# Optimization experiments

Measured on AMD Instinct MI355X. Metric: run time of the kernel, lower is better.

Reference implementation:

```python
import jax, jax.numpy as jnp
import numpy as np

B, S, D, H, P = 4, 512, 512, 8, 16
DK = D // H  # 64


def setup_inputs() -> dict:
    k0 = jax.random.key(0)
    ks = jax.random.split(k0, 10)
    std = 0.02
    lin = lambda k, shape: jax.random.normal(k, shape, dtype=jnp.float32) * std
    inp = {}
    inp["query"] = jax.random.normal(ks[0], (B, S, D), dtype=jnp.float32)
    inp["key"] = jax.random.normal(ks[1], (B, S, D), dtype=jnp.float32)
    inp["value"] = jax.random.normal(ks[2], (B, S, D), dtype=jnp.float32)
    inp["Wq"] = lin(ks[3], (D, D)); inp["bq"] = jnp.zeros((D,), jnp.float32)
    inp["Wk"] = lin(ks[4], (D, D)); inp["bk"] = jnp.zeros((D,), jnp.float32)
    inp["Wv"] = lin(ks[5], (D, D)); inp["bv"] = jnp.zeros((D,), jnp.float32)
    inp["Wo"] = lin(ks[6], (D, D)); inp["bo"] = jnp.zeros((D,), jnp.float32)
    inp["rel_table"] = lin(ks[7], (2 * P + 1, DK))  # nn.Embedding(2P+1, d_k)
    inp["gamma"] = jnp.ones((D,), jnp.float32)
    inp["beta"] = jnp.zeros((D,), jnp.float32)
    inp["mask"] = jnp.ones((B, S), dtype=jnp.int32)
    inp["relative_positions"] = jax.random.randint(ks[8], (B, S, S, DK), -32, 33, dtype=jnp.int32)
    return inp


def reference(query, key, value, Wq, bq, Wk, bk, Wv, bv, Wo, bo, rel_table, gamma, beta, mask, relative_positions):
    b, s, d = query.shape
    dk = rel_table.shape[1]
    h = d // dk
    pmax = (rel_table.shape[0] - 1) // 2

    def heads(x, W, bias):
        return (x @ W.T + bias).reshape(b, s, h, dk).transpose(0, 2, 1, 3)  # [b,h,s,dk]

    Q = heads(query, Wq, bq)
    K = heads(key, Wk, bk)
    V = heads(value, Wv, bv)

    scores = jnp.einsum('bhid,bhjd->bhij', Q, K) / jnp.sqrt(jnp.float32(dk))

    # torch: einsum('bhid,bijde->bhije', Q, emb(idx)).mean(-1)
    # mean over e commutes with the d-contraction -> pre-average the table.
    idx = jnp.clip(relative_positions, -pmax, pmax) + pmax  # [b,i,j,d]
    bias_d = rel_table.mean(axis=-1)[idx]                   # [b,i,j,d]
    scores = scores + jnp.einsum('bhid,bijd->bhij', Q, bias_d)

    scores = jnp.where(mask[:, None, None, :] == 0, jnp.float32(-1e9), scores)
    attn = jax.nn.softmax(scores, axis=-1)  # dropout is identity in eval

    ctx = jnp.einsum('bhij,bhjd->bhid', attn, V).transpose(0, 2, 1, 3).reshape(b, s, d)
    out = ctx @ Wo.T + bo

    x = out + query  # residual
    mu = x.mean(-1, keepdims=True)
    var = x.var(-1, keepdims=True)
    y = (x - mu) / jnp.sqrt(var + 1e-5) * gamma + beta
    return (y, attn)
```

## Files before the change

### kernel.cpp

```cpp
#include <hip/hip_runtime.h>
#include <hip/hip_bf16.h>

#define BB 4
#define SS 512
#define DD 512
#define HH 8
#define DK 64
#define PP 16
#define TSZ 33

typedef __bf16 bf16x8 __attribute__((ext_vector_type(8)));
typedef float  f32x4  __attribute__((ext_vector_type(4)));

__device__ inline bf16x8 cvt8(const float* __restrict__ p) {
    f32x4 a = *(const f32x4*)p;
    f32x4 b = *(const f32x4*)(p + 4);
    bf16x8 r;
    r[0] = (__bf16)a[0]; r[1] = (__bf16)a[1]; r[2] = (__bf16)a[2]; r[3] = (__bf16)a[3];
    r[4] = (__bf16)b[0]; r[5] = (__bf16)b[1]; r[6] = (__bf16)b[2]; r[7] = (__bf16)b[3];
    return r;
}

__global__ void tmean_kernel(const float* __restrict__ rel_table, float* __restrict__ Tm) {
    int t = threadIdx.x;
    if (t < TSZ) {
        float s = 0.f;
        for (int e = 0; e < DK; ++e) s += rel_table[t * DK + e];
        Tm[t] = s * (1.f / DK);
    }
}

__global__ void proj_mfma_kernel(const float* __restrict__ X, const float* __restrict__ W,
                                 const float* __restrict__ bias, __bf16* __restrict__ out,
                                 int mode) {
    int lane = threadIdx.x;
    int wave = threadIdx.y;
    int tm = blockIdx.y * 4 + wave;
    int tn = blockIdx.x;
    int m = lane & 15, quad = lane >> 4;

    const float* arow = X + (size_t)(tm * 16 + m) * DD + quad * 8;
    const float* brow = W + (size_t)(tn * 16 + m) * DD + quad * 8;

    f32x4 acc = {0.f, 0.f, 0.f, 0.f};
    for (int k0 = 0; k0 < DD; k0 += 32) {
        bf16x8 a = cvt8(arow + k0);
        bf16x8 b = cvt8(brow + k0);
        acc = __builtin_amdgcn_mfma_f32_16x16x32_bf16(a, b, acc, 0, 0, 0);
    }

    int col = tn * 16 + m;
    int h = col >> 6, dk = col & (DK - 1);
    float bv = bias[col];
#pragma unroll
    for (int r = 0; r < 4; ++r) {
        int rowg = tm * 16 + quad * 4 + r;
        int b = rowg >> 9, i = rowg & (SS - 1);
        float v = acc[r] + bv;
        if (mode == 0)
            out[((size_t)(b * HH + h) * SS + i) * DK + dk] = (__bf16)v;
        else
            out[((size_t)(b * HH + h) * DK + dk) * SS + i] = (__bf16)v;
    }
}

__global__ void scores_mfma_kernel(const __bf16* __restrict__ Q, const __bf16* __restrict__ K,
                                   float* __restrict__ scores) {
    int bh = blockIdx.z;
    int lane = threadIdx.x, wave = threadIdx.y;
    int tm = blockIdx.y * 4 + wave;
    int tn = blockIdx.x;
    int m = lane & 15, quad = lane >> 4;

    const __bf16* qrow = Q + ((size_t)bh * SS + tm * 16 + m) * DK + quad * 8;
    const __bf16* krow = K + ((size_t)bh * SS + tn * 16 + m) * DK + quad * 8;

    f32x4 acc = {0.f, 0.f, 0.f, 0.f};
#pragma unroll
    for (int k0 = 0; k0 < DK; k0 += 32) {
        bf16x8 a = *(const bf16x8*)(qrow + k0);
        bf16x8 b = *(const bf16x8*)(krow + k0);
        acc = __builtin_amdgcn_mfma_f32_16x16x32_bf16(a, b, acc, 0, 0, 0);
    }

    int col = tn * 16 + m;
#pragma unroll
    for (int r = 0; r < 4; ++r) {
        int rowg = tm * 16 + quad * 4 + r;
        scores[((size_t)bh * SS + rowg) * SS + col] = acc[r] * 0.125f;
    }
}

__global__ void relbias_kernel(const __bf16* __restrict__ Q, const int* __restrict__ relpos,
                               const float* __restrict__ Tm, float* __restrict__ scores) {
    int b = blockIdx.z;
    int i = blockIdx.y;
    int j0 = blockIdx.x * 64;
    __shared__ float tmean[TSZ];
    __shared__ float qrow[DD];
    int t = threadIdx.x;
    if (t < TSZ) tmean[t] = Tm[t];
    for (int o = t; o < DD; o += 256) {
        int h = o >> 6, d = o & (DK - 1);
        qrow[o] = (float)Q[((size_t)(b * HH + h) * SS + i) * DK + d];
    }
    __syncthreads();
    int jl = t >> 2, qq = t & 3;
    int j = j0 + jl;
    const int4* ip4 = (const int4*)(relpos + (((size_t)(b * SS + i) * SS + j) * DK) + qq * 16);
    int4 w0 = ip4[0], w1 = ip4[1], w2 = ip4[2], w3 = ip4[3];
    int rr[16] = {w0.x, w0.y, w0.z, w0.w, w1.x, w1.y, w1.z, w1.w,
                  w2.x, w2.y, w2.z, w2.w, w3.x, w3.y, w3.z, w3.w};
    float tv[16];
#pragma unroll
    for (int kk = 0; kk < 16; ++kk) {
        int r = min(max(rr[kk], -PP), PP) + PP;
        tv[kk] = tmean[r];
    }
#pragma unroll
    for (int h = 0; h < HH; ++h) {
        float p = 0.f;
#pragma unroll
        for (int kk = 0; kk < 16; ++kk) p += qrow[h * DK + qq * 16 + kk] * tv[kk];
        p += __shfl_xor(p, 1);
        p += __shfl_xor(p, 2);
        if (qq == 0) scores[((size_t)(b * HH + h) * SS + i) * SS + j] += p;
    }
}

__global__ void softmax_kernel(float* __restrict__ attn, const int* __restrict__ mask) {
    int bhi = blockIdx.x;
    int b = bhi >> 12;
    float* row = attn + (size_t)bhi * SS;
    int t = threadIdx.x;
    float v0 = row[t];
    float v1 = row[t + 256];
    if (mask[b * SS + t] == 0) v0 = -1e9f;
    if (mask[b * SS + t + 256] == 0) v1 = -1e9f;

    __shared__ float red[4];
    float m = fmaxf(v0, v1);
#pragma unroll
    for (int off = 32; off >= 1; off >>= 1) m = fmaxf(m, __shfl_xor(m, off));
    if ((t & 63) == 0) red[t >> 6] = m;
    __syncthreads();
    float mall = fmaxf(fmaxf(red[0], red[1]), fmaxf(red[2], red[3]));
    __syncthreads();

    float e0 = expf(v0 - mall);
    float e1 = expf(v1 - mall);
    float s = e0 + e1;
#pragma unroll
    for (int off = 32; off >= 1; off >>= 1) s += __shfl_xor(s, off);
    if ((t & 63) == 0) red[t >> 6] = s;
    __syncthreads();
    float sall = red[0] + red[1] + red[2] + red[3];
    float inv = 1.f / sall;
    row[t] = e0 * inv;
    row[t + 256] = e1 * inv;
}

__global__ void ctx_mfma_kernel(const float* __restrict__ attn, const __bf16* __restrict__ Vt,
                                __bf16* __restrict__ ctx_bsd) {
    int bh = blockIdx.z;
    int bb = bh >> 3, h = bh & 7;
    int lane = threadIdx.x, wave = threadIdx.y;
    int tm = blockIdx.y * 4 + wave;
    int tn = blockIdx.x;
    int m = lane & 15, quad = lane >> 4;

    const float*  arow = attn + ((size_t)bh * SS + tm * 16 + m) * SS + quad * 8;
    const __bf16* brow = Vt + ((size_t)bh * DK + tn * 16 + m) * SS + quad * 8;

    f32x4 acc = {0.f, 0.f, 0.f, 0.f};
    for (int k0 = 0; k0 < SS; k0 += 32) {
        bf16x8 a = cvt8(arow + k0);
        bf16x8 b = *(const bf16x8*)(brow + k0);
        acc = __builtin_amdgcn_mfma_f32_16x16x32_bf16(a, b, acc, 0, 0, 0);
    }

    int d = tn * 16 + m;
#pragma unroll
    for (int r = 0; r < 4; ++r) {
        int i = tm * 16 + quad * 4 + r;
        ctx_bsd[((size_t)(bb * SS + i)) * DD + h * DK + d] = (__bf16)acc[r];
    }
}

__global__ void outproj_mfma_kernel(const __bf16* __restrict__ Xc, const float* __restrict__ Wo,
                                    const float* __restrict__ bo, const float* __restrict__ query,
                                    float* __restrict__ xres) {
    int lane = threadIdx.x, wave = threadIdx.y;
    int tm = blockIdx.y * 4 + wave;
    int tn = blockIdx.x;
    int m = lane & 15, quad = lane >> 4;

    const __bf16* arow = Xc + (size_t)(tm * 16 + m) * DD + quad * 8;
    const float*  brow = Wo + (size_t)(tn * 16 + m) * DD + quad * 8;

    f32x4 acc = {0.f, 0.f, 0.f, 0.f};
    for (int k0 = 0; k0 < DD; k0 += 32) {
        bf16x8 a = *(const bf16x8*)(arow + k0);
        bf16x8 b = cvt8(brow + k0);
        acc = __builtin_amdgcn_mfma_f32_16x16x32_bf16(a, b, acc, 0, 0, 0);
    }

    int col = tn * 16 + m;
    float bv = bo[col];
#pragma unroll
    for (int r = 0; r < 4; ++r) {
        int rowg = tm * 16 + quad * 4 + r;
        xres[(size_t)rowg * DD + col] = acc[r] + bv + query[(size_t)rowg * DD + col];
    }
}

__global__ void ln_kernel(const float* __restrict__ x, const float* __restrict__ gamma,
                          const float* __restrict__ beta, float* __restrict__ y) {
    int r = blockIdx.x;
    int t = threadIdx.x;
    float v0 = x[r * DD + t];
    float v1 = x[r * DD + t + 256];
    __shared__ float red[4];
    float s = v0 + v1;
#pragma unroll
    for (int off = 32; off >= 1; off >>= 1) s += __shfl_xor(s, off);
    if ((t & 63) == 0) red[t >> 6] = s;
    __syncthreads();
    float mu = (red[0] + red[1] + red[2] + red[3]) * (1.f / DD);
    __syncthreads();
    float d0 = v0 - mu, d1 = v1 - mu;
    float sq = d0 * d0 + d1 * d1;
#pragma unroll
    for (int off = 32; off >= 1; off >>= 1) sq += __shfl_xor(sq, off);
    if ((t & 63) == 0) red[t >> 6] = sq;
    __syncthreads();
    float var = (red[0] + red[1] + red[2] + red[3]) * (1.f / DD);
    float inv = rsqrtf(var + 1e-5f);
    y[r * DD + t] = d0 * inv * gamma[t] + beta[t];
    y[r * DD + t + 256] = d1 * inv * gamma[t + 256] + beta[t + 256];
}

extern "C" void kernel_launch(void* const* d_in, const int* in_sizes, int n_in,
                              void* d_out, int out_size, void* d_ws, size_t ws_size,
                              hipStream_t stream) {
    const float* query  = (const float*)d_in[0];
    const float* key    = (const float*)d_in[1];
    const float* value  = (const float*)d_in[2];
    const float* Wq     = (const float*)d_in[3];
    const float* bq     = (const float*)d_in[4];
    const float* Wk     = (const float*)d_in[5];
    const float* bk     = (const float*)d_in[6];
    const float* Wv     = (const float*)d_in[7];
    const float* bv     = (const float*)d_in[8];
    const float* Wo     = (const float*)d_in[9];
    const float* bo     = (const float*)d_in[10];
    const float* rtab   = (const float*)d_in[11];
    const float* gamma  = (const float*)d_in[12];
    const float* beta   = (const float*)d_in[13];
    const int*   mask   = (const int*)d_in[14];
    const int*   relpos = (const int*)d_in[15];

    float* out = (float*)d_out;
    float* y    = out;
    float* attn = out + (size_t)BB * SS * DD;

    char* wsb = (char*)d_ws;
    float*  Tm    = (float*)wsb;                       wsb += 256;
    __bf16* Qbf   = (__bf16*)wsb;                      wsb += (size_t)BB * HH * SS * DK * 2;
    __bf16* Kbf   = (__bf16*)wsb;                      wsb += (size_t)BB * HH * SS * DK * 2;
    __bf16* Vtbf  = (__bf16*)wsb;                      wsb += (size_t)BB * HH * DK * SS * 2;
    __bf16* ctxbf = (__bf16*)wsb;                      wsb += (size_t)BB * SS * DD * 2;
    float*  xres  = (float*)wsb;                       wsb += (size_t)BB * SS * DD * 4;

    hipLaunchKernelGGL(tmean_kernel, dim3(1), dim3(64), 0, stream, rtab, Tm);

    dim3 wblk(64, 4);
    dim3 gproj(DD / 16, (BB * SS) / 64);
    hipLaunchKernelGGL(proj_mfma_kernel, gproj, wblk, 0, stream, query, Wq, bq, Qbf, 0);
    hipLaunchKernelGGL(proj_mfma_kernel, gproj, wblk, 0, stream, key,   Wk, bk, Kbf, 0);
    hipLaunchKernelGGL(proj_mfma_kernel, gproj, wblk, 0, stream, value, Wv, bv, Vtbf, 1);

    hipLaunchKernelGGL(scores_mfma_kernel, dim3(SS / 16, SS / 64, BB * HH), wblk, 0, stream,
                       Qbf, Kbf, attn);

    hipLaunchKernelGGL(relbias_kernel, dim3(SS / 64, SS, BB), dim3(256), 0, stream,
                       Qbf, relpos, Tm, attn);

    hipLaunchKernelGGL(softmax_kernel, dim3(BB * HH * SS), dim3(256), 0, stream, attn, mask);

    hipLaunchKernelGGL(ctx_mfma_kernel, dim3(DK / 16, SS / 64, BB * HH), wblk, 0, stream,
                       attn, Vtbf, ctxbf);

    hipLaunchKernelGGL(outproj_mfma_kernel, gproj, wblk, 0, stream, ctxbf, Wo, bo, query, xres);

    hipLaunchKernelGGL(ln_kernel, dim3(BB * SS), dim3(256), 0, stream, xres, gamma, beta, y);
}
```

Measured before the change: 581.0 us.

## Fuse scores, relative bias, mask and partial softmax; fuse normalize with context GEMM

Merges the three Q/K/V projection launches into one grid over z. Scores, the relative-position bias (relpos gathered through LDS), masking and a per-128-column partial softmax now run in one kernel that writes unnormalized exponentials plus per-chunk max and sum. A second kernel combines the partial statistics, rescales and writes the attention rows, and feeds them from LDS into the attention-times-V MFMA. This removes several full read-modify-write passes over the large scores tensor. In exchange it adds extra synchronisation, heavy LDS use, and the bias dot products now use bf16 table values.

```diff
diff --git a/kernel.cpp b/kernel.cpp
--- a/kernel.cpp
+++ b/kernel.cpp
@@ -10,6 +10,7 @@
 #define TSZ 33
 
 typedef __bf16 bf16x8 __attribute__((ext_vector_type(8)));
+typedef __bf16 bf16x4 __attribute__((ext_vector_type(4)));
 typedef float  f32x4  __attribute__((ext_vector_type(4)));
 
 __device__ inline bf16x8 cvt8(const float* __restrict__ p) {
@@ -30,11 +31,22 @@
     }
 }
 
-__global__ void proj_mfma_kernel(const float* __restrict__ X, const float* __restrict__ W,
-                                 const float* __restrict__ bias, __bf16* __restrict__ out,
-                                 int mode) {
-    int lane = threadIdx.x;
-    int wave = threadIdx.y;
+__global__ void proj_mfma_kernel(const float* __restrict__ X0, const float* __restrict__ X1,
+                                 const float* __restrict__ X2,
+                                 const float* __restrict__ W0, const float* __restrict__ W1,
+                                 const float* __restrict__ W2,
+                                 const float* __restrict__ B0, const float* __restrict__ B1,
+                                 const float* __restrict__ B2,
+                                 __bf16* __restrict__ O0, __bf16* __restrict__ O1,
+                                 __bf16* __restrict__ O2) {
+    int z = blockIdx.z;
+    const float* X = (z == 0) ? X0 : (z == 1) ? X1 : X2;
+    const float* W = (z == 0) ? W0 : (z == 1) ? W1 : W2;
+    const float* bias = (z == 0) ? B0 : (z == 1) ? B1 : B2;
+    __bf16* out = (z == 0) ? O0 : (z == 1) ? O1 : O2;
+    int mode = (z == 2);
+
+    int lane = threadIdx.x, wave = threadIdx.y;
     int tm = blockIdx.y * 4 + wave;
     int tn = blockIdx.x;
     int m = lane & 15, quad = lane >> 4;
@@ -64,126 +76,199 @@
     }
 }
 
-__global__ void scores_mfma_kernel(const __bf16* __restrict__ Q, const __bf16* __restrict__ K,
-                                   float* __restrict__ scores) {
-    int bh = blockIdx.z;
-    int lane = threadIdx.x, wave = threadIdx.y;
-    int tm = blockIdx.y * 4 + wave;
-    int tn = blockIdx.x;
-    int m = lane & 15, quad = lane >> 4;
-
-    const __bf16* qrow = Q + ((size_t)bh * SS + tm * 16 + m) * DK + quad * 8;
-    const __bf16* krow = K + ((size_t)bh * SS + tn * 16 + m) * DK + quad * 8;
-
+__launch_bounds__(512, 2)
+__global__ void f1_kernel(const __bf16* __restrict__ Qbf, const __bf16* __restrict__ Kbf,
+                          const int* __restrict__ relpos, const float* __restrict__ Tm,
+                          const int* __restrict__ mask, float* __restrict__ attn,
+                          float* __restrict__ pm, float* __restrict__ pl) {
+    __shared__ __bf16 tm_sh[16 * 16 * 72];
+    __shared__ __bf16 qs_sh[8 * 17 * 72];
+    __shared__ float  bias_sh[8 * 16 * 17];
+    __shared__ float  tmean_sh[TSZ];
+
+    int l = threadIdx.x, w = threadIdx.y;
+    int t = w * 64 + l;
+    int jq = blockIdx.x, i0 = blockIdx.y, b = blockIdx.z;
+
+    if (t < TSZ) tmean_sh[t] = Tm[t];
+
+    {
+        int f = t * 16;
+        int h = f >> 10, i = (f >> 6) & 15, d0 = f & 63;
+        const __bf16* src = Qbf + ((size_t)(b * HH + h) * SS + i0 * 16 + i) * DK + d0;
+        bf16x8 v0 = *(const bf16x8*)src;
+        bf16x8 v1 = *(const bf16x8*)(src + 8);
+        *(bf16x8*)&qs_sh[(h * 17 + i) * 72 + d0] = v0;
+        *(bf16x8*)&qs_sh[(h * 17 + i) * 72 + d0 + 8] = v1;
+    }
+
+    int m = l & 15, quad = l >> 4;
+    const __bf16* qrow = Qbf + ((size_t)(b * HH + w) * SS + i0 * 16 + m) * DK + quad * 8;
+    bf16x8 a0 = *(const bf16x8*)qrow;
+    bf16x8 a1 = *(const bf16x8*)(qrow + 32);
+
+    f32x4 acc[8];
+#pragma unroll
+    for (int jt = 0; jt < 8; ++jt) {
+        const __bf16* krow = Kbf + ((size_t)(b * HH + w) * SS + jq * 128 + jt * 16 + m) * DK + quad * 8;
+        bf16x8 b0 = *(const bf16x8*)krow;
+        bf16x8 b1 = *(const bf16x8*)(krow + 32);
+        f32x4 c = {0.f, 0.f, 0.f, 0.f};
+        c = __builtin_amdgcn_mfma_f32_16x16x32_bf16(a0, b0, c, 0, 0, 0);
+        c = __builtin_amdgcn_mfma_f32_16x16x32_bf16(a1, b1, c, 0, 0, 0);
+        acc[jt] = c;
+    }
+
+    int h8 = l & 7, j8 = l >> 3;
+
+    for (int jt = 0; jt < 8; ++jt) {
+        __syncthreads();
+        const int* gidx = relpos + ((size_t)(b * SS + i0 * 16) * SS + jq * 128 + jt * 16) * DK;
+#pragma unroll
+        for (int c = 0; c < 8; ++c) {
+            int f = c * 2048 + t * 4;
+            int i = f >> 10, rem = f & 1023;
+            int4 v = *(const int4*)(gidx + (size_t)i * (SS * DK) + rem);
+            int j = rem >> 6, d = rem & 63;
+            int c0 = min(max(v.x, -PP), PP) + PP;
+            int c1 = min(max(v.y, -PP), PP) + PP;
+            int c2 = min(max(v.z, -PP), PP) + PP;
+            int c3 = min(max(v.w, -PP), PP) + PP;
+            bf16x4 pk = {(__bf16)tmean_sh[c0], (__bf16)tmean_sh[c1],
+                         (__bf16)tmean_sh[c2], (__bf16)tmean_sh[c3]};
+            *(bf16x4*)&tm_sh[(i * 16 + j) * 72 + d] = pk;
+        }
+        __syncthreads();
+#pragma unroll
+        for (int ii = 0; ii < 2; ++ii) {
+            int i = w * 2 + ii;
+#pragma unroll
+            for (int half = 0; half < 2; ++half) {
+                int j = j8 + 8 * half;
+                float bacc = 0.f;
+#pragma unroll
+                for (int d8 = 0; d8 < 8; ++d8) {
+                    bf16x8 tv = *(bf16x8*)&tm_sh[(i * 16 + j) * 72 + d8 * 8];
+                    bf16x8 qv = *(bf16x8*)&qs_sh[(h8 * 17 + i) * 72 + d8 * 8];
+#pragma unroll
+                    for (int k = 0; k < 8; ++k) bacc += (float)tv[k] * (float)qv[k];
+                }
+                bias_sh[(h8 * 16 + i) * 17 + j] = bacc;
+            }
+        }
+        __syncthreads();
+#pragma unroll
+        for (int r = 0; r < 4; ++r)
+            acc[jt][r] = acc[jt][r] * 0.125f + bias_sh[(w * 16 + quad * 4 + r) * 17 + m];
+    }
+
+#pragma unroll
+    for (int jt = 0; jt < 8; ++jt) {
+        int mv = mask[b * SS + jq * 128 + jt * 16 + m];
+        if (mv == 0) {
+#pragma unroll
+            for (int r = 0; r < 4; ++r) acc[jt][r] = -1e9f;
+        }
+    }
+
+#pragma unroll
+    for (int r = 0; r < 4; ++r) {
+        float mx = -1e30f;
+#pragma unroll
+        for (int jt = 0; jt < 8; ++jt) mx = fmaxf(mx, acc[jt][r]);
+        mx = fmaxf(mx, __shfl_xor(mx, 1));
+        mx = fmaxf(mx, __shfl_xor(mx, 2));
+        mx = fmaxf(mx, __shfl_xor(mx, 4));
+        mx = fmaxf(mx, __shfl_xor(mx, 8));
+        float sum = 0.f;
+#pragma unroll
+        for (int jt = 0; jt < 8; ++jt) {
+            float e = __expf(acc[jt][r] - mx);
+            acc[jt][r] = e;
+            sum += e;
+        }
+        sum += __shfl_xor(sum, 1);
+        sum += __shfl_xor(sum, 2);
+        sum += __shfl_xor(sum, 4);
+        sum += __shfl_xor(sum, 8);
+        if (m == 0) {
+            int row = i0 * 16 + quad * 4 + r;
+            pm[((size_t)(b * HH + w) * SS + row) * 4 + jq] = mx;
+            pl[((size_t)(b * HH + w) * SS + row) * 4 + jq] = sum;
+        }
+    }
+
+#pragma unroll
+    for (int jt = 0; jt < 8; ++jt) {
+#pragma unroll
+        for (int r = 0; r < 4; ++r) {
+            attn[((size_t)(b * HH + w) * SS + i0 * 16 + quad * 4 + r) * SS
+                 + jq * 128 + jt * 16 + m] = acc[jt][r];
+        }
+    }
+}
+
+__launch_bounds__(256, 4)
+__global__ void f2_kernel(float* __restrict__ attn, const float* __restrict__ pm,
+                          const float* __restrict__ pl, const __bf16* __restrict__ Vt,
+                          __bf16* __restrict__ ctx_bsd) {
+    __shared__ float scl[4][16];
+    __shared__ __bf16 p_sh[16 * 520];
+
+    int t = threadIdx.x;
+    int l = t & 63, wv = t >> 6;
+    int i0 = blockIdx.x, bh = blockIdx.y;
+
+    if (t < 16) {
+        int row = i0 * 16 + t;
+        float m0 = pm[((size_t)bh * SS + row) * 4 + 0];
+        float m1 = pm[((size_t)bh * SS + row) * 4 + 1];
+        float m2 = pm[((size_t)bh * SS + row) * 4 + 2];
+        float m3 = pm[((size_t)bh * SS + row) * 4 + 3];
+        float l0 = pl[((size_t)bh * SS + row) * 4 + 0];
+        float l1 = pl[((size_t)bh * SS + row) * 4 + 1];
+        float l2 = pl[((size_t)bh * SS + row) * 4 + 2];
+        float l3 = pl[((size_t)bh * SS + row) * 4 + 3];
+        float M = fmaxf(fmaxf(m0, m1), fmaxf(m2, m3));
+        float e0 = __expf(m0 - M), e1 = __expf(m1 - M);
+        float e2 = __expf(m2 - M), e3 = __expf(m3 - M);
+        float L = l0 * e0 + l1 * e1 + l2 * e2 + l3 * e3;
+        float inv = 1.f / L;
+        scl[0][t] = e0 * inv; scl[1][t] = e1 * inv;
+        scl[2][t] = e2 * inv; scl[3][t] = e3 * inv;
+    }
+    __syncthreads();
+
+    float* arow = attn + ((size_t)bh * SS + i0 * 16) * SS;
+#pragma unroll
+    for (int rr = 0; rr < 4; ++rr) {
+        int row = wv * 4 + rr;
+#pragma unroll
+        for (int it = 0; it < 2; ++it) {
+            int col = it * 256 + l * 4;
+            f32x4 v = *(f32x4*)(arow + (size_t)row * SS + col);
+            float s = scl[col >> 7][row];
+            v[0] *= s; v[1] *= s; v[2] *= s; v[3] *= s;
+            *(f32x4*)(arow + (size_t)row * SS + col) = v;
+            bf16x4 pk = {(__bf16)v[0], (__bf16)v[1], (__bf16)v[2], (__bf16)v[3]};
+            *(bf16x4*)&p_sh[row * 520 + col] = pk;
+        }
+    }
+    __syncthreads();
+
+    int m = l & 15, quad = l >> 4;
     f32x4 acc = {0.f, 0.f, 0.f, 0.f};
-#pragma unroll
-    for (int k0 = 0; k0 < DK; k0 += 32) {
-        bf16x8 a = *(const bf16x8*)(qrow + k0);
-        bf16x8 b = *(const bf16x8*)(krow + k0);
-        acc = __builtin_amdgcn_mfma_f32_16x16x32_bf16(a, b, acc, 0, 0, 0);
-    }
-
-    int col = tn * 16 + m;
+    const __bf16* vrow = Vt + ((size_t)bh * DK + wv * 16 + m) * SS + quad * 8;
+    for (int k0 = 0; k0 < SS; k0 += 32) {
+        bf16x8 aF = *(bf16x8*)&p_sh[m * 520 + k0 + quad * 8];
+        bf16x8 bF = *(const bf16x8*)(vrow + k0);
+        acc = __builtin_amdgcn_mfma_f32_16x16x32_bf16(aF, bF, acc, 0, 0, 0);
+    }
+    int b = bh >> 3, h = bh & 7;
 #pragma unroll
     for (int r = 0; r < 4; ++r) {
-        int rowg = tm * 16 + quad * 4 + r;
-        scores[((size_t)bh * SS + rowg) * SS + col] = acc[r] * 0.125f;
-    }
-}
-
-__global__ void relbias_kernel(const __bf16* __restrict__ Q, const int* __restrict__ relpos,
-                               const float* __restrict__ Tm, float* __restrict__ scores) {
-    int b = blockIdx.z;
-    int i = blockIdx.y;
-    int j0 = blockIdx.x * 64;
-    __shared__ float tmean[TSZ];
-    __shared__ float qrow[DD];
-    int t = threadIdx.x;
-    if (t < TSZ) tmean[t] = Tm[t];
-    for (int o = t; o < DD; o += 256) {
-        int h = o >> 6, d = o & (DK - 1);
-        qrow[o] = (float)Q[((size_t)(b * HH + h) * SS + i) * DK + d];
-    }
-    __syncthreads();
-    int jl = t >> 2, qq = t & 3;
-    int j = j0 + jl;
-    const int4* ip4 = (const int4*)(relpos + (((size_t)(b * SS + i) * SS + j) * DK) + qq * 16);
-    int4 w0 = ip4[0], w1 = ip4[1], w2 = ip4[2], w3 = ip4[3];
-    int rr[16] = {w0.x, w0.y, w0.z, w0.w, w1.x, w1.y, w1.z, w1.w,
-                  w2.x, w2.y, w2.z, w2.w, w3.x, w3.y, w3.z, w3.w};
-    float tv[16];
-#pragma unroll
-    for (int kk = 0; kk < 16; ++kk) {
-        int r = min(max(rr[kk], -PP), PP) + PP;
-        tv[kk] = tmean[r];
-    }
-#pragma unroll
-    for (int h = 0; h < HH; ++h) {
-        float p = 0.f;
-#pragma unroll
-        for (int kk = 0; kk < 16; ++kk) p += qrow[h * DK + qq * 16 + kk] * tv[kk];
-        p += __shfl_xor(p, 1);
-        p += __shfl_xor(p, 2);
-        if (qq == 0) scores[((size_t)(b * HH + h) * SS + i) * SS + j] += p;
-    }
-}
-
-__global__ void softmax_kernel(float* __restrict__ attn, const int* __restrict__ mask) {
-    int bhi = blockIdx.x;
-    int b = bhi >> 12;
-    float* row = attn + (size_t)bhi * SS;
-    int t = threadIdx.x;
-    float v0 = row[t];
-    float v1 = row[t + 256];
-    if (mask[b * SS + t] == 0) v0 = -1e9f;
-    if (mask[b * SS + t + 256] == 0) v1 = -1e9f;
-
-    __shared__ float red[4];
-    float m = fmaxf(v0, v1);
-#pragma unroll
-    for (int off = 32; off >= 1; off >>= 1) m = fmaxf(m, __shfl_xor(m, off));
-    if ((t & 63) == 0) red[t >> 6] = m;
-    __syncthreads();
-    float mall = fmaxf(fmaxf(red[0], red[1]), fmaxf(red[2], red[3]));
-    __syncthreads();
-
-    float e0 = expf(v0 - mall);
-    float e1 = expf(v1 - mall);
-    float s = e0 + e1;
-#pragma unroll
-    for (int off = 32; off >= 1; off >>= 1) s += __shfl_xor(s, off);
-    if ((t & 63) == 0) red[t >> 6] = s;
-    __syncthreads();
-    float sall = red[0] + red[1] + red[2] + red[3];
-    float inv = 1.f / sall;
-    row[t] = e0 * inv;
-    row[t + 256] = e1 * inv;
-}
-
-__global__ void ctx_mfma_kernel(const float* __restrict__ attn, const __bf16* __restrict__ Vt,
-                                __bf16* __restrict__ ctx_bsd) {
-    int bh = blockIdx.z;
-    int bb = bh >> 3, h = bh & 7;
-    int lane = threadIdx.x, wave = threadIdx.y;
-    int tm = blockIdx.y * 4 + wave;
-    int tn = blockIdx.x;
-    int m = lane & 15, quad = lane >> 4;
-
-    const float*  arow = attn + ((size_t)bh * SS + tm * 16 + m) * SS + quad * 8;
-    const __bf16* brow = Vt + ((size_t)bh * DK + tn * 16 + m) * SS + quad * 8;
-
-    f32x4 acc = {0.f, 0.f, 0.f, 0.f};
-    for (int k0 = 0; k0 < SS; k0 += 32) {
-        bf16x8 a = cvt8(arow + k0);
-        bf16x8 b = *(const bf16x8*)(brow + k0);
-        acc = __builtin_amdgcn_mfma_f32_16x16x32_bf16(a, b, acc, 0, 0, 0);
-    }
-
-    int d = tn * 16 + m;
-#pragma unroll
-    for (int r = 0; r < 4; ++r) {
-        int i = tm * 16 + quad * 4 + r;
-        ctx_bsd[((size_t)(bb * SS + i)) * DD + h * DK + d] = (__bf16)acc[r];
+        ctx_bsd[((size_t)(b * SS + i0 * 16 + quad * 4 + r)) * DD + h * DK + wv * 16 + m]
+            = (__bf16)acc[r];
     }
 }
 
@@ -265,33 +350,29 @@
     float* attn = out + (size_t)BB * SS * DD;
 
     char* wsb = (char*)d_ws;
-    float*  Tm    = (float*)wsb;                       wsb += 256;
-    __bf16* Qbf   = (__bf16*)wsb;                      wsb += (size_t)BB * HH * SS * DK * 2;
-    __bf16* Kbf   = (__bf16*)wsb;                      wsb += (size_t)BB * HH * SS * DK * 2;
-    __bf16* Vtbf  = (__bf16*)wsb;                      wsb += (size_t)BB * HH * DK * SS * 2;
-    __bf16* ctxbf = (__bf16*)wsb;                      wsb += (size_t)BB * SS * DD * 2;
-    float*  xres  = (float*)wsb;                       wsb += (size_t)BB * SS * DD * 4;
+    float*  Tm    = (float*)wsb;   wsb += 256;
+    __bf16* Qbf   = (__bf16*)wsb;  wsb += (size_t)BB * HH * SS * DK * 2;
+    __bf16* Kbf   = (__bf16*)wsb;  wsb += (size_t)BB * HH * SS * DK * 2;
+    __bf16* Vtbf  = (__bf16*)wsb;  wsb += (size_t)BB * HH * DK * SS * 2;
+    __bf16* ctxbf = (__bf16*)wsb;  wsb += (size_t)BB * SS * DD * 2;
+    float*  xres  = (float*)wsb;   wsb += (size_t)BB * SS * DD * 4;
+    float*  pm    = (float*)wsb;   wsb += (size_t)BB * HH * SS * 4 * 4;
+    float*  pl    = (float*)wsb;   wsb += (size_t)BB * HH * SS * 4 * 4;
 
     hipLaunchKernelGGL(tmean_kernel, dim3(1), dim3(64), 0, stream, rtab, Tm);
 
     dim3 wblk(64, 4);
-    dim3 gproj(DD / 16, (BB * SS) / 64);
-    hipLaunchKernelGGL(proj_mfma_kernel, gproj, wblk, 0, stream, query, Wq, bq, Qbf, 0);
-    hipLaunchKernelGGL(proj_mfma_kernel, gproj, wblk, 0, stream, key,   Wk, bk, Kbf, 0);
-    hipLaunchKernelGGL(proj_mfma_kernel, gproj, wblk, 0, stream, value, Wv, bv, Vtbf, 1);
-
-    hipLaunchKernelGGL(scores_mfma_kernel, dim3(SS / 16, SS / 64, BB * HH), wblk, 0, stream,
-                       Qbf, Kbf, attn);
-
-    hipLaunchKernelGGL(relbias_kernel, dim3(SS / 64, SS, BB), dim3(256), 0, stream,
-                       Qbf, relpos, Tm, attn);
-
-    hipLaunchKernelGGL(softmax_kernel, dim3(BB * HH * SS), dim3(256), 0, stream, attn, mask);
-
-    hipLaunchKernelGGL(ctx_mfma_kernel, dim3(DK / 16, SS / 64, BB * HH), wblk, 0, stream,
-                       attn, Vtbf, ctxbf);
-
-    hipLaunchKernelGGL(outproj_mfma_kernel, gproj, wblk, 0, stream, ctxbf, Wo, bo, query, xres);
+    hipLaunchKernelGGL(proj_mfma_kernel, dim3(DD / 16, (BB * SS) / 64, 3), wblk, 0, stream,
+                       query, key, value, Wq, Wk, Wv, bq, bk, bv, Qbf, Kbf, Vtbf);
+
+    hipLaunchKernelGGL(f1_kernel, dim3(4, SS / 16, BB), dim3(64, 8), 0, stream,
+                       Qbf, Kbf, relpos, Tm, mask, attn, pm, pl);
+
+    hipLaunchKernelGGL(f2_kernel, dim3(SS / 16, BB * HH), dim3(256), 0, stream,
+                       attn, pm, pl, Vtbf, ctxbf);
+
+    hipLaunchKernelGGL(outproj_mfma_kernel, dim3(DD / 16, (BB * SS) / 64), wblk, 0, stream,
+                       ctxbf, Wo, bo, query, xres);
 
     hipLaunchKernelGGL(ln_kernel, dim3(BB * SS), dim3(256), 0, stream, xres, gamma, beta, y);
 }
```

Measured after the change: 581.5 us. No clear change (+0.1%).
